# Kernel optimization log

Hardware: AMD Instinct MI355X
Metric: run time of the kernel (lower is better)

Reference implementation:

```python
import jax, jax.numpy as jnp
import numpy as np

NF = 64        # num_feat
B = 4
H = 128
W = 128
KH = KW = 3
K = KH * KW    # 9 kernel taps
DG = 1         # deformable_groups


def conv3x3(x, w, b):
    y = jax.lax.conv_general_dilated(
        x, w, window_strides=(1, 1), padding=((1, 1), (1, 1)),
        dimension_numbers=('NCHW', 'OIHW', 'NCHW'))
    return y + b[None, :, None, None]


def lrelu(x):
    return jnp.where(x >= 0, x, 0.1 * x)


def modulated_deform_conv(x, offset, mask, w, b):
    """DCNv2: bilinear gather at learned offsets, modulated by sigmoid mask.
    x: [B,C,H,W], offset: [B,2K,H,W] (y,x interleaved per tap), mask: [B,K,H,W].
    stride=1, padding=1, dilation=1, zero outside boundaries (mmcv semantics).
    """
    Bb, C, Hh, Ww = x.shape
    off = offset.reshape(Bb, K, 2, Hh, Ww)
    oy, ox = off[:, :, 0], off[:, :, 1]
    ki = (jnp.arange(K) // KW - 1).astype(x.dtype)  # dilation*i - pad
    kj = (jnp.arange(K) % KW - 1).astype(x.dtype)
    py = jnp.arange(Hh, dtype=x.dtype)[None, None, :, None] + ki[None, :, None, None] + oy  # [B,K,H,W]
    px = jnp.arange(Ww, dtype=x.dtype)[None, None, None, :] + kj[None, :, None, None] + ox
    y0 = jnp.floor(py)
    x0 = jnp.floor(px)
    wy1 = py - y0
    wx1 = px - x0
    x_flat = x.reshape(Bb, C, Hh * Ww)

    def gather(yi, xi):
        valid = (yi >= 0) & (yi < Hh) & (xi >= 0) & (xi < Ww)
        yc = jnp.clip(yi, 0, Hh - 1).astype(jnp.int32)
        xc = jnp.clip(xi, 0, Ww - 1).astype(jnp.int32)
        idx = (yc * Ww + xc).reshape(Bb, -1)                      # [B, K*H*W]
        g = jax.vmap(lambda xf, i: jnp.take(xf, i, axis=1))(x_flat, idx)  # [B,C,K*H*W]
        g = g.reshape(Bb, C, K, Hh, Ww)
        return g * valid[:, None].astype(x.dtype)

    v00 = gather(y0, x0)
    v01 = gather(y0, x0 + 1)
    v10 = gather(y0 + 1, x0)
    v11 = gather(y0 + 1, x0 + 1)
    wy = wy1[:, None]
    wx = wx1[:, None]
    samp = (v00 * (1 - wy) * (1 - wx) + v01 * (1 - wy) * wx
            + v10 * wy * (1 - wx) + v11 * wy * wx)                # [B,C,K,H,W]
    samp = samp * mask[:, None]
    out = jnp.einsum('bckhw,ock->bohw', samp, w.reshape(w.shape[0], C, K))
    return out + b[None, :, None, None]


def setup_inputs() -> dict:
    key = jax.random.key(0)
    ks = jax.random.split(key, 12)
    s = 0.05
    return {
        'nbr_feat_l': jax.random.normal(ks[0], (B, NF, H, W), jnp.float32),
        'ref_feat_l': jax.random.normal(ks[1], (B, NF, H, W), jnp.float32),
        'w1': jax.random.normal(ks[2], (NF, 2 * NF, 3, 3), jnp.float32) * s,
        'b1': jnp.zeros((NF,), jnp.float32),
        'w2': jax.random.normal(ks[3], (NF, NF, 3, 3), jnp.float32) * s,
        'b2': jnp.zeros((NF,), jnp.float32),
        'w3': jax.random.normal(ks[4], (NF, NF, 3, 3), jnp.float32) * s,
        'b3': jnp.zeros((NF,), jnp.float32),
        'w_off': jax.random.normal(ks[5], (DG * 3 * K, NF, 3, 3), jnp.float32) * s,
        'b_off': jnp.zeros((DG * 3 * K,), jnp.float32),
        'w_dcn': jax.random.normal(ks[6], (NF, NF, 3, 3), jnp.float32) * s,
        'b_dcn': jnp.zeros((NF,), jnp.float32),
    }


def reference(nbr_feat_l, ref_feat_l, w1, b1, w2, b2, w3, b3, w_off, b_off, w_dcn, b_dcn):
    o = jnp.concatenate([nbr_feat_l, ref_feat_l], axis=1)
    o = lrelu(conv3x3(o, w1, b1))
    o = lrelu(conv3x3(o, w2, b2))
    o = lrelu(conv3x3(o, w3, b3))
    out = conv3x3(o, w_off, b_off)                      # [B, 27, H, W]
    o1, o2, m = jnp.split(out, 3, axis=1)
    offset = 15 * jnp.tanh(jnp.concatenate([o1, o2], axis=1))  # [B, 18, H, W]
    mask = jax.nn.sigmoid(m)                                   # [B, 9, H, W]
    feat = lrelu(modulated_deform_conv(nbr_feat_l, offset, mask, w_dcn, b_dcn))
    return feat, offset, mask
```

## Files before the change

kernel.cpp:

```cpp
#include <hip/hip_runtime.h>
#include <math.h>


typedef _Float16 h8 __attribute__((ext_vector_type(8)));
typedef _Float16 h4 __attribute__((ext_vector_type(4)));
typedef _Float16 h2 __attribute__((ext_vector_type(2)));
typedef float f4 __attribute__((ext_vector_type(4)));

__global__ __launch_bounds__(256) void setup_kernel(
    const float* __restrict__ nbr, const float* __restrict__ refp,
    const float* __restrict__ w1, const float* __restrict__ w2,
    const float* __restrict__ w3, const float* __restrict__ w_off,
    const float* __restrict__ w_dcn,
    _Float16* __restrict__ X1, _Float16* __restrict__ X2,
    _Float16* __restrict__ B64, _Float16* __restrict__ C64,
    _Float16* __restrict__ wF1, _Float16* __restrict__ wF2,
    _Float16* __restrict__ wF3, _Float16* __restrict__ wFo,
    _Float16* __restrict__ wFd) {
  __shared__ float t[64 * 65];
  int bid = blockIdx.x;
  int tid = threadIdx.x;
  if (bid < 792) {
    int i = bid * 256 + tid;
    if (i < 73728) {
      int j = i;
      int icw = j & 31; int t1 = j >> 5; int oc = t1 & 63; int t2 = t1 >> 6;
      int ch = t2 & 3; int tap = t2 >> 2; int ic = ch * 32 + icw;
      wF1[j] = (_Float16)w1[(oc * 128 + ic) * 9 + tap];
    } else if (i < 110592) {
      int j = i - 73728;
      int icw = j & 31; int t1 = j >> 5; int oc = t1 & 63; int t2 = t1 >> 6;
      int ch = t2 & 1; int tap = t2 >> 1; int ic = ch * 32 + icw;
      wF2[j] = (_Float16)w2[(oc * 64 + ic) * 9 + tap];
    } else if (i < 147456) {
      int j = i - 110592;
      int icw = j & 31; int t1 = j >> 5; int oc = t1 & 63; int t2 = t1 >> 6;
      int ch = t2 & 1; int tap = t2 >> 1; int ic = ch * 32 + icw;
      wF3[j] = (_Float16)w3[(oc * 64 + ic) * 9 + tap];
    } else if (i < 165888) {
      int j = i - 147456;
      int icw = j & 31; int t1 = j >> 5; int oc = t1 & 31; int t2 = t1 >> 5;
      int ch = t2 & 1; int tap = t2 >> 1; int ic = ch * 32 + icw;
      float v = (oc < 27) ? w_off[(oc * 64 + ic) * 9 + tap] : 0.f;
      wFo[j] = (_Float16)v;
    } else if (i < 202752) {
      int j = i - 165888;
      int oc = j / 576; int r = j - oc * 576; int tap = r >> 6; int c = r & 63;
      wFd[j] = (_Float16)w_dcn[(oc * 64 + c) * 9 + tap];
    }
    return;
  }
  if (bid < 1050) {
    int i = (bid - 792) * 256 + tid;
    int bufi = i / 16512;
    int j = i - bufi * 16512;
    int b = j / 4128;
    int r = j - b * 4128;
    int p = r >> 3; int cg = r & 7;
    int row, col;
    if (p < 130)      { row = 0;   col = p; }
    else if (p < 260) { row = 129; col = p - 130; }
    else if (p < 388) { row = 1 + (p - 260); col = 0; }
    else              { row = 1 + (p - 388); col = 129; }
    _Float16* dst = (bufi == 0) ? X1 : (bufi == 1) ? X2 : (bufi == 2) ? B64 : C64;
    uint4 z; z.x = z.y = z.z = z.w = 0u;
    *(uint4*)(dst + ((size_t)(b * 130 + row) * 130 + col) * 64 + cg * 8) = z;
    return;
  }
  int j = bid - 1050;
  int half = j & 1;
  int y = (j >> 1) & 127;
  int b = (j >> 8) & 3;
  int src = j >> 10;
  const float* sp = src ? refp : nbr;
  _Float16* dst = src ? X2 : X1;
  for (int l = tid; l < 64 * 64; l += 256) {
    int c = l >> 6, gx = l & 63;
    t[c * 65 + gx] = sp[(((size_t)b * 64 + c) << 14) + (y << 7) + half * 64 + gx];
  }
  __syncthreads();
  unsigned* dstU = (unsigned*)dst;
  for (int l = tid; l < 64 * 32; l += 256) {
    int pxl = l >> 5, c2 = l & 31;
    union { _Float16 h[2]; unsigned u; } pk;
    pk.h[0] = (_Float16)t[(2 * c2) * 65 + pxl];
    pk.h[1] = (_Float16)t[(2 * c2 + 1) * 65 + pxl];
    dstU[((size_t)(b * 130 + y + 1) * 130 + 1 + half * 64 + pxl) * 32 + c2] = pk.u;
  }
}

template <int NCH, bool SPLIT>
__global__ __launch_bounds__(128, 1) void conv3x3_w64_kernel(
    const _Float16* __restrict__ X1, const _Float16* __restrict__ X2,
    const _Float16* __restrict__ W, const float* __restrict__ bias,
    _Float16* __restrict__ outP) {
  int tid = threadIdx.x;
  int wv = tid >> 6, L = tid & 63;
  int lm = L & 15, lq = L >> 4;
  int bid = blockIdx.x;
  int xcd = bid & 7, j = bid >> 3;
  int y = (xcd << 4) | (j & 15);
  int b = j >> 4;
  int px0 = wv * 64;

  f4 acc[4][4];
#pragma unroll
  for (int i = 0; i < 4; ++i)
#pragma unroll
    for (int n = 0; n < 4; ++n) acc[i][n] = (f4)0.f;

#pragma unroll
  for (int c = 0; c < NCH; ++c) {
    const _Float16* src = (SPLIT && c >= 2) ? X2 : X1;
    int cl = SPLIT ? (c & 1) : c;
#pragma unroll
    for (int tap = 0; tap < 9; ++tap) {
      const int dy = tap / 3 - 1, dx = tap % 3 - 1;
      const _Float16* xb = src + ((size_t)((b * 130 + (y + 1 + dy)) * 130) + (1 + dx) + px0) * 64
                               + cl * 32 + lq * 8;
      h8 b0 = *(const h8*)(xb + lm * 64);
      h8 b1 = *(const h8*)(xb + (16 + lm) * 64);
      h8 b2 = *(const h8*)(xb + (32 + lm) * 64);
      h8 b3 = *(const h8*)(xb + (48 + lm) * 64);
      const _Float16* wp = W + (size_t)((tap * NCH + c) * 64) * 32 + lm * 32 + lq * 8;
      h8 a0 = *(const h8*)(wp);
      h8 a1 = *(const h8*)(wp + 512);
      h8 a2 = *(const h8*)(wp + 1024);
      h8 a3 = *(const h8*)(wp + 1536);
#pragma unroll
      for (int mt = 0; mt < 4; ++mt) {
        h8 am = (mt == 0) ? a0 : (mt == 1) ? a1 : (mt == 2) ? a2 : a3;
        acc[mt][0] = __builtin_amdgcn_mfma_f32_16x16x32_f16(am, b0, acc[mt][0], 0, 0, 0);
        acc[mt][1] = __builtin_amdgcn_mfma_f32_16x16x32_f16(am, b1, acc[mt][1], 0, 0, 0);
        acc[mt][2] = __builtin_amdgcn_mfma_f32_16x16x32_f16(am, b2, acc[mt][2], 0, 0, 0);
        acc[mt][3] = __builtin_amdgcn_mfma_f32_16x16x32_f16(am, b3, acc[mt][3], 0, 0, 0);
      }
    }
  }
  const size_t obase = ((size_t)(b * 130 + (y + 1)) * 130 + 1) * 64;
#pragma unroll
  for (int mt = 0; mt < 4; ++mt)
#pragma unroll
    for (int nt = 0; nt < 4; ++nt) {
      int px = px0 + nt * 16 + lm;
      h4 pk;
#pragma unroll
      for (int r = 0; r < 4; ++r) {
        int oc = mt * 16 + lq * 4 + r;
        float v = acc[mt][nt][r] + bias[oc];
        v = (v >= 0.f) ? v : 0.1f * v;
        pk[r] = (_Float16)v;
      }
      *(h4*)(outP + obase + (size_t)px * 64 + mt * 16 + lq * 4) = pk;
    }
}

__global__ __launch_bounds__(256, 8) void off_dcn_kernel(
    const _Float16* __restrict__ Xc, const _Float16* __restrict__ Xs,
    const _Float16* __restrict__ Wo, const float* __restrict__ bo,
    const _Float16* __restrict__ wD, const float* __restrict__ bd,
    float* __restrict__ off_out, float* __restrict__ mask_out,
    float* __restrict__ out) {
  __shared__ _Float16 S[32 * 200];
  __shared__ float Soff[32][28];
  int tid = threadIdx.x;
  int wv = tid >> 6, L = tid & 63;
  int lm = L & 15, lq = L >> 4;
  int t8 = L >> 3, c8 = L & 7;
  int g = blockIdx.x;
  int xcd = g & 7;
  int r0 = g >> 3;
  int q = r0 & 3;
  int y = (xcd << 4) | ((r0 >> 2) & 15);
  int b = r0 >> 6;
  int pxq0 = q * 32;

  if (wv < 2) {
    int px0 = pxq0 + wv * 16;
    f4 oa[2];
    oa[0] = (f4)0.f; oa[1] = (f4)0.f;
#pragma unroll
    for (int c = 0; c < 2; ++c)
#pragma unroll
      for (int tap = 0; tap < 9; ++tap) {
        const int dy = tap / 3 - 1, dx = tap % 3 - 1;
        const _Float16* xb = Xc + ((size_t)((b * 130 + (y + 1 + dy)) * 130) + (1 + dx) + px0) * 64
                                + c * 32 + lq * 8;
        h8 b0 = *(const h8*)(xb + lm * 64);
        const _Float16* wp = Wo + (size_t)((tap * 2 + c) * 32 + lm) * 32 + lq * 8;
        h8 a0 = *(const h8*)(wp);
        h8 a1 = *(const h8*)(wp + 512);
        oa[0] = __builtin_amdgcn_mfma_f32_16x16x32_f16(a0, b0, oa[0], 0, 0, 0);
        oa[1] = __builtin_amdgcn_mfma_f32_16x16x32_f16(a1, b0, oa[1], 0, 0, 0);
      }
    int gpx = px0 + lm;
    int hw = (y << 7) + gpx;
    int lpx = wv * 16 + lm;
#pragma unroll
    for (int mt = 0; mt < 2; ++mt)
#pragma unroll
      for (int r = 0; r < 4; ++r) {
        int oc = mt * 16 + lq * 4 + r;
        if (oc < 18) {
          float v = 15.f * tanhf(oa[mt][r] + bo[oc]);
          off_out[((b * 18 + oc) << 14) + hw] = v;
          Soff[lpx][oc] = v;
        } else if (oc < 27) {
          float v = 1.f / (1.f + expf(-(oa[mt][r] + bo[oc])));
          mask_out[((b * 9 + (oc - 18)) << 14) + hw] = v;
          Soff[lpx][oc] = v;
        }
      }
  }

  f4 acc[2];
  acc[0] = (f4)0.f; acc[1] = (f4)0.f;
  int wvM = wv >> 1, wvN = wv & 1;

#pragma unroll
  for (int p = 0; p < 3; ++p) {
    const int tap0 = p * 3;
    __syncthreads();
#pragma unroll
    for (int it = 0; it < 3; ++it) {
      int u = it * 32 + wv * 8 + t8;
      int px = u & 31;
      int tl = u >> 5;
      int k = tap0 + tl;
      int wg = pxq0 + px;
      int kr = k / 3;
      float oy = Soff[px][2 * k];
      float ox = Soff[px][2 * k + 1];
      float m = Soff[px][18 + k];
      float py = (float)(y + kr - 1) + oy;
      float pxf = (float)(wg + (k - kr * 3) - 1) + ox;
      float fy = floorf(py), fx = floorf(pxf);
      float wy = py - fy, wx = pxf - fx;
      int y0 = (int)fy, x0 = (int)fx;
      int y1 = y0 + 1, x1 = x0 + 1;
      float vy0 = ((unsigned)y0 < 128u) ? 1.f : 0.f;
      float vy1 = ((unsigned)y1 < 128u) ? 1.f : 0.f;
      float vx0 = ((unsigned)x0 < 128u) ? 1.f : 0.f;
      float vx1 = ((unsigned)x1 < 128u) ? 1.f : 0.f;
      float ey = 1.f - wy, ex = 1.f - wx;
      _Float16 w00 = (_Float16)(ey * ex * m * vy0 * vx0);
      _Float16 w01 = (_Float16)(ey * wx * m * vy0 * vx1);
      _Float16 w10 = (_Float16)(wy * ex * m * vy1 * vx0);
      _Float16 w11 = (_Float16)(wy * wx * m * vy1 * vx1);
      h2 W00 = {w00, w00}, W01 = {w01, w01}, W10 = {w10, w10}, W11 = {w11, w11};
      int y0c = min(max(y0, 0), 127) + 1, y1c = min(max(y1, 0), 127) + 1;
      int x0c = min(max(x0, 0), 127) + 1, x1c = min(max(x1, 0), 127) + 1;
      int rb = b * 130;
      h8 v00 = *(const h8*)(Xs + ((size_t)((rb + y0c) * 130 + x0c) << 6) + c8 * 8);
      h8 v01 = *(const h8*)(Xs + ((size_t)((rb + y0c) * 130 + x1c) << 6) + c8 * 8);
      h8 v10 = *(const h8*)(Xs + ((size_t)((rb + y1c) * 130 + x0c) << 6) + c8 * 8);
      h8 v11 = *(const h8*)(Xs + ((size_t)((rb + y1c) * 130 + x1c) << 6) + c8 * 8);
      h8 o;
#pragma unroll
      for (int j2 = 0; j2 < 4; ++j2) {
        h2 a = {v00[2 * j2], v00[2 * j2 + 1]};
        h2 bb = {v01[2 * j2], v01[2 * j2 + 1]};
        h2 cc = {v10[2 * j2], v10[2 * j2 + 1]};
        h2 dd = {v11[2 * j2], v11[2 * j2 + 1]};
        h2 r = a * W00;
        r += bb * W01;
        r += cc * W10;
        r += dd * W11;
        o[2 * j2] = r[0];
        o[2 * j2 + 1] = r[1];
      }
      *(h8*)&S[px * 200 + tl * 64 + c8 * 8] = o;
    }
    __syncthreads();
#pragma unroll
    for (int ks = 0; ks < 6; ++ks) {
      int kg = tap0 * 64 + ks * 32;
      const _Float16* wp = wD + (size_t)(wvM * 32 + lm) * 576 + kg + lq * 8;
      h8 a0 = *(const h8*)(wp);
      h8 a1 = *(const h8*)(wp + 16 * 576);
      h8 bv = *(const h8*)(&S[(wvN * 16 + lm) * 200 + ks * 32 + lq * 8]);
      acc[0] = __builtin_amdgcn_mfma_f32_16x16x32_f16(a0, bv, acc[0], 0, 0, 0);
      acc[1] = __builtin_amdgcn_mfma_f32_16x16x32_f16(a1, bv, acc[1], 0, 0, 0);
    }
  }
  int px = pxq0 + wvN * 16 + lm;
#pragma unroll
  for (int mt = 0; mt < 2; ++mt)
#pragma unroll
    for (int r = 0; r < 4; ++r) {
      int oc = wvM * 32 + mt * 16 + lq * 4 + r;
      float v = acc[mt][r] + bd[oc];
      v = (v >= 0.f) ? v : 0.1f * v;
      out[(((b << 6) + oc) << 14) + (y << 7) + px] = v;
    }
}

extern "C" void kernel_launch(void* const* d_in, const int* in_sizes, int n_in,
                              void* d_out, int out_size, void* d_ws, size_t ws_size,
                              hipStream_t stream) {
  const float* nbr   = (const float*)d_in[0];
  const float* refp  = (const float*)d_in[1];
  const float* w1    = (const float*)d_in[2];
  const float* b1    = (const float*)d_in[3];
  const float* w2    = (const float*)d_in[4];
  const float* b2    = (const float*)d_in[5];
  const float* w3    = (const float*)d_in[6];
  const float* b3    = (const float*)d_in[7];
  const float* w_off = (const float*)d_in[8];
  const float* b_off = (const float*)d_in[9];
  const float* w_dcn = (const float*)d_in[10];
  const float* b_dcn = (const float*)d_in[11];

  float* outp = (float*)d_out;
  float* feat = outp;
  float* offp = outp + 4194304;
  float* mskp = outp + 4194304 + 1179648;

  char* ws = (char*)d_ws;
  const size_t PB = 8652800;
  _Float16* X1  = (_Float16*)ws;
  _Float16* X2  = (_Float16*)(ws + PB);
  _Float16* B64 = (_Float16*)(ws + 2 * PB);
  _Float16* C64 = (_Float16*)(ws + 3 * PB);
  char* p = ws + 4 * PB;
  _Float16* wF1 = (_Float16*)p;  p += (size_t)73728 * 2;
  _Float16* wF2 = (_Float16*)p;  p += (size_t)36864 * 2;
  _Float16* wF3 = (_Float16*)p;  p += (size_t)36864 * 2;
  _Float16* wFo = (_Float16*)p;  p += (size_t)18432 * 2;
  _Float16* wFd = (_Float16*)p;

  setup_kernel<<<dim3(3098), 256, 0, stream>>>(nbr, refp, w1, w2, w3, w_off, w_dcn,
                                               X1, X2, B64, C64, wF1, wF2, wF3, wFo, wFd);
  conv3x3_w64_kernel<4, true><<<dim3(512), 128, 0, stream>>>(X1, X2, wF1, b1, B64);
  conv3x3_w64_kernel<2, false><<<dim3(512), 128, 0, stream>>>(B64, nullptr, wF2, b2, C64);
  conv3x3_w64_kernel<2, false><<<dim3(512), 128, 0, stream>>>(C64, nullptr, wF3, b3, B64);
  off_dcn_kernel<<<dim3(2048), 256, 0, stream>>>(B64, X1, wFo, b_off, wFd, b_dcn,
                                                 offp, mskp, feat);
}
```

Baseline: 228.9 us.

## Split conv output channels across blocks and spread offset conv over all waves

The three 3x3 conv kernels now split the 64 output channels into two halves per block and use four waves of 32 pixels each. This doubles the grid to 1024 blocks of 256 threads, with a 2x2 MFMA tile per wave instead of 4x4. The offset/mask conv in the fused DCN kernel is now spread across all four waves, each computing one 16-channel half for 16 pixels, instead of only two waves doing both halves. The goal is more parallelism and occupancy and less register pressure per wave. The cost is less data reuse per wave, so input pixels and weights are loaded more often. The launch-bounds occupancy hint on the DCN kernel is also lowered.

```diff
diff --git a/kernel.cpp b/kernel.cpp
--- a/kernel.cpp
+++ b/kernel.cpp
@@ -90,7 +90,7 @@
 }
 
 template <int NCH, bool SPLIT>
-__global__ __launch_bounds__(128, 1) void conv3x3_w64_kernel(
+__global__ __launch_bounds__(256, 4) void conv3x3_w32_kernel(
     const _Float16* __restrict__ X1, const _Float16* __restrict__ X2,
     const _Float16* __restrict__ W, const float* __restrict__ bias,
     _Float16* __restrict__ outP) {
@@ -99,15 +99,16 @@
   int lm = L & 15, lq = L >> 4;
   int bid = blockIdx.x;
   int xcd = bid & 7, j = bid >> 3;
-  int y = (xcd << 4) | (j & 15);
-  int b = j >> 4;
-  int px0 = wv * 64;
-
-  f4 acc[4][4];
-#pragma unroll
-  for (int i = 0; i < 4; ++i)
-#pragma unroll
-    for (int n = 0; n < 4; ++n) acc[i][n] = (f4)0.f;
+  int och = j & 1;
+  int y = (xcd << 4) | ((j >> 1) & 15);
+  int b = j >> 5;
+  int px0 = wv * 32;
+
+  f4 acc[2][2];
+#pragma unroll
+  for (int i = 0; i < 2; ++i)
+#pragma unroll
+    for (int n = 0; n < 2; ++n) acc[i][n] = (f4)0.f;
 
 #pragma unroll
   for (int c = 0; c < NCH; ++c) {
@@ -120,42 +121,34 @@
                                + cl * 32 + lq * 8;
       h8 b0 = *(const h8*)(xb + lm * 64);
       h8 b1 = *(const h8*)(xb + (16 + lm) * 64);
-      h8 b2 = *(const h8*)(xb + (32 + lm) * 64);
-      h8 b3 = *(const h8*)(xb + (48 + lm) * 64);
-      const _Float16* wp = W + (size_t)((tap * NCH + c) * 64) * 32 + lm * 32 + lq * 8;
+      const _Float16* wp = W + (size_t)((tap * NCH + c) * 64 + och * 32 + lm) * 32 + lq * 8;
       h8 a0 = *(const h8*)(wp);
       h8 a1 = *(const h8*)(wp + 512);
-      h8 a2 = *(const h8*)(wp + 1024);
-      h8 a3 = *(const h8*)(wp + 1536);
-#pragma unroll
-      for (int mt = 0; mt < 4; ++mt) {
-        h8 am = (mt == 0) ? a0 : (mt == 1) ? a1 : (mt == 2) ? a2 : a3;
-        acc[mt][0] = __builtin_amdgcn_mfma_f32_16x16x32_f16(am, b0, acc[mt][0], 0, 0, 0);
-        acc[mt][1] = __builtin_amdgcn_mfma_f32_16x16x32_f16(am, b1, acc[mt][1], 0, 0, 0);
-        acc[mt][2] = __builtin_amdgcn_mfma_f32_16x16x32_f16(am, b2, acc[mt][2], 0, 0, 0);
-        acc[mt][3] = __builtin_amdgcn_mfma_f32_16x16x32_f16(am, b3, acc[mt][3], 0, 0, 0);
-      }
+      acc[0][0] = __builtin_amdgcn_mfma_f32_16x16x32_f16(a0, b0, acc[0][0], 0, 0, 0);
+      acc[0][1] = __builtin_amdgcn_mfma_f32_16x16x32_f16(a0, b1, acc[0][1], 0, 0, 0);
+      acc[1][0] = __builtin_amdgcn_mfma_f32_16x16x32_f16(a1, b0, acc[1][0], 0, 0, 0);
+      acc[1][1] = __builtin_amdgcn_mfma_f32_16x16x32_f16(a1, b1, acc[1][1], 0, 0, 0);
     }
   }
   const size_t obase = ((size_t)(b * 130 + (y + 1)) * 130 + 1) * 64;
 #pragma unroll
-  for (int mt = 0; mt < 4; ++mt)
-#pragma unroll
-    for (int nt = 0; nt < 4; ++nt) {
+  for (int mt = 0; mt < 2; ++mt)
+#pragma unroll
+    for (int nt = 0; nt < 2; ++nt) {
       int px = px0 + nt * 16 + lm;
       h4 pk;
 #pragma unroll
       for (int r = 0; r < 4; ++r) {
-        int oc = mt * 16 + lq * 4 + r;
+        int oc = och * 32 + mt * 16 + lq * 4 + r;
         float v = acc[mt][nt][r] + bias[oc];
         v = (v >= 0.f) ? v : 0.1f * v;
         pk[r] = (_Float16)v;
       }
-      *(h4*)(outP + obase + (size_t)px * 64 + mt * 16 + lq * 4) = pk;
+      *(h4*)(outP + obase + (size_t)px * 64 + och * 32 + mt * 16 + lq * 4) = pk;
     }
 }
 
-__global__ __launch_bounds__(256, 8) void off_dcn_kernel(
+__global__ __launch_bounds__(256, 4) void off_dcn_kernel(
     const _Float16* __restrict__ Xc, const _Float16* __restrict__ Xs,
     const _Float16* __restrict__ Wo, const float* __restrict__ bo,
     const _Float16* __restrict__ wD, const float* __restrict__ bd,
@@ -175,10 +168,10 @@
   int b = r0 >> 6;
   int pxq0 = q * 32;
 
-  if (wv < 2) {
-    int px0 = pxq0 + wv * 16;
-    f4 oa[2];
-    oa[0] = (f4)0.f; oa[1] = (f4)0.f;
+  {
+    int pxh = wv & 1, oh = wv >> 1;
+    int px0 = pxq0 + pxh * 16;
+    f4 oa = (f4)0.f;
 #pragma unroll
     for (int c = 0; c < 2; ++c)
 #pragma unroll
@@ -187,30 +180,26 @@
         const _Float16* xb = Xc + ((size_t)((b * 130 + (y + 1 + dy)) * 130) + (1 + dx) + px0) * 64
                                 + c * 32 + lq * 8;
         h8 b0 = *(const h8*)(xb + lm * 64);
-        const _Float16* wp = Wo + (size_t)((tap * 2 + c) * 32 + lm) * 32 + lq * 8;
+        const _Float16* wp = Wo + (size_t)((tap * 2 + c) * 32 + oh * 16 + lm) * 32 + lq * 8;
         h8 a0 = *(const h8*)(wp);
-        h8 a1 = *(const h8*)(wp + 512);
-        oa[0] = __builtin_amdgcn_mfma_f32_16x16x32_f16(a0, b0, oa[0], 0, 0, 0);
-        oa[1] = __builtin_amdgcn_mfma_f32_16x16x32_f16(a1, b0, oa[1], 0, 0, 0);
+        oa = __builtin_amdgcn_mfma_f32_16x16x32_f16(a0, b0, oa, 0, 0, 0);
       }
     int gpx = px0 + lm;
     int hw = (y << 7) + gpx;
-    int lpx = wv * 16 + lm;
-#pragma unroll
-    for (int mt = 0; mt < 2; ++mt)
-#pragma unroll
-      for (int r = 0; r < 4; ++r) {
-        int oc = mt * 16 + lq * 4 + r;
-        if (oc < 18) {
-          float v = 15.f * tanhf(oa[mt][r] + bo[oc]);
-          off_out[((b * 18 + oc) << 14) + hw] = v;
-          Soff[lpx][oc] = v;
-        } else if (oc < 27) {
-          float v = 1.f / (1.f + expf(-(oa[mt][r] + bo[oc])));
-          mask_out[((b * 9 + (oc - 18)) << 14) + hw] = v;
-          Soff[lpx][oc] = v;
-        }
+    int lpx = pxh * 16 + lm;
+#pragma unroll
+    for (int r = 0; r < 4; ++r) {
+      int oc = oh * 16 + lq * 4 + r;
+      if (oc < 18) {
+        float v = 15.f * tanhf(oa[r] + bo[oc]);
+        off_out[((b * 18 + oc) << 14) + hw] = v;
+        Soff[lpx][oc] = v;
+      } else if (oc < 27) {
+        float v = 1.f / (1.f + expf(-(oa[r] + bo[oc])));
+        mask_out[((b * 9 + (oc - 18)) << 14) + hw] = v;
+        Soff[lpx][oc] = v;
       }
+    }
   }
 
   f4 acc[2];
@@ -331,9 +320,9 @@
 
   setup_kernel<<<dim3(3098), 256, 0, stream>>>(nbr, refp, w1, w2, w3, w_off, w_dcn,
                                                X1, X2, B64, C64, wF1, wF2, wF3, wFo, wFd);
-  conv3x3_w64_kernel<4, true><<<dim3(512), 128, 0, stream>>>(X1, X2, wF1, b1, B64);
-  conv3x3_w64_kernel<2, false><<<dim3(512), 128, 0, stream>>>(B64, nullptr, wF2, b2, C64);
-  conv3x3_w64_kernel<2, false><<<dim3(512), 128, 0, stream>>>(C64, nullptr, wF3, b3, B64);
+  conv3x3_w32_kernel<4, true><<<dim3(1024), 256, 0, stream>>>(X1, X2, wF1, b1, B64);
+  conv3x3_w32_kernel<2, false><<<dim3(1024), 256, 0, stream>>>(B64, nullptr, wF2, b2, C64);
+  conv3x3_w32_kernel<2, false><<<dim3(1024), 256, 0, stream>>>(C64, nullptr, wF3, b3, B64);
   off_dcn_kernel<<<dim3(2048), 256, 0, stream>>>(B64, X1, wFo, b_off, wFd, b_dcn,
                                                  offp, mskp, feat);
 }
```

New measurement: 274.1 us. 1.2x slower.

## Fuse DCN sampling directly into MFMA operands per wave, removing shared staging

Applied to the files above, without the earlier changes.

Each block now covers 64 pixels, and every wave owns 16 of them end to end. The wave computes the offset conv for its pixels, then builds the bilinear-sampled B operand in registers and feeds it straight into MFMAs over all 64 output channels. This removes the shared-memory sample tile and the block-wide barriers between sampling and the GEMM, and all four waves now do offset-conv work instead of two. The cost is more accumulators per wave (4 f4 instead of 2), which is why launch bounds drop to 4 blocks per CU. The grid is also halved, so there is less parallelism to hide gather latency.

```diff
diff --git a/kernel.cpp b/kernel.cpp
--- a/kernel.cpp
+++ b/kernel.cpp
@@ -155,28 +155,29 @@
     }
 }
 
-__global__ __launch_bounds__(256, 8) void off_dcn_kernel(
+__global__ __launch_bounds__(256, 4) void off_dcn_kernel(
     const _Float16* __restrict__ Xc, const _Float16* __restrict__ Xs,
     const _Float16* __restrict__ Wo, const float* __restrict__ bo,
     const _Float16* __restrict__ wD, const float* __restrict__ bd,
     float* __restrict__ off_out, float* __restrict__ mask_out,
     float* __restrict__ out) {
-  __shared__ _Float16 S[32 * 200];
-  __shared__ float Soff[32][28];
+  __shared__ float Soff[4][16][28];
   int tid = threadIdx.x;
   int wv = tid >> 6, L = tid & 63;
   int lm = L & 15, lq = L >> 4;
-  int t8 = L >> 3, c8 = L & 7;
+  int lq8 = lq * 8;
   int g = blockIdx.x;
   int xcd = g & 7;
   int r0 = g >> 3;
-  int q = r0 & 3;
-  int y = (xcd << 4) | ((r0 >> 2) & 15);
-  int b = r0 >> 6;
-  int pxq0 = q * 32;
-
-  if (wv < 2) {
-    int px0 = pxq0 + wv * 16;
+  int half = r0 & 1;
+  int y = (xcd << 4) | ((r0 >> 1) & 15);
+  int b = r0 >> 5;
+  int px0 = half * 64 + wv * 16;
+  int gpx = px0 + lm;
+  int hw = (y << 7) + gpx;
+  int rb = b * 130;
+
+  {
     f4 oa[2];
     oa[0] = (f4)0.f; oa[1] = (f4)0.f;
 #pragma unroll
@@ -184,18 +185,15 @@
 #pragma unroll
       for (int tap = 0; tap < 9; ++tap) {
         const int dy = tap / 3 - 1, dx = tap % 3 - 1;
-        const _Float16* xb = Xc + ((size_t)((b * 130 + (y + 1 + dy)) * 130) + (1 + dx) + px0) * 64
-                                + c * 32 + lq * 8;
+        const _Float16* xb = Xc + ((size_t)((rb + (y + 1 + dy)) * 130) + (1 + dx) + px0) * 64
+                                + c * 32 + lq8;
         h8 b0 = *(const h8*)(xb + lm * 64);
-        const _Float16* wp = Wo + (size_t)((tap * 2 + c) * 32 + lm) * 32 + lq * 8;
+        const _Float16* wp = Wo + (size_t)((tap * 2 + c) * 32 + lm) * 32 + lq8;
         h8 a0 = *(const h8*)(wp);
         h8 a1 = *(const h8*)(wp + 512);
         oa[0] = __builtin_amdgcn_mfma_f32_16x16x32_f16(a0, b0, oa[0], 0, 0, 0);
         oa[1] = __builtin_amdgcn_mfma_f32_16x16x32_f16(a1, b0, oa[1], 0, 0, 0);
       }
-    int gpx = px0 + lm;
-    int hw = (y << 7) + gpx;
-    int lpx = wv * 16 + lm;
 #pragma unroll
     for (int mt = 0; mt < 2; ++mt)
 #pragma unroll
@@ -204,61 +202,57 @@
         if (oc < 18) {
           float v = 15.f * tanhf(oa[mt][r] + bo[oc]);
           off_out[((b * 18 + oc) << 14) + hw] = v;
-          Soff[lpx][oc] = v;
+          Soff[wv][lm][oc] = v;
         } else if (oc < 27) {
           float v = 1.f / (1.f + expf(-(oa[mt][r] + bo[oc])));
           mask_out[((b * 9 + (oc - 18)) << 14) + hw] = v;
-          Soff[lpx][oc] = v;
+          Soff[wv][lm][oc] = v;
         }
       }
   }
 
-  f4 acc[2];
-  acc[0] = (f4)0.f; acc[1] = (f4)0.f;
-  int wvM = wv >> 1, wvN = wv & 1;
-
-#pragma unroll
-  for (int p = 0; p < 3; ++p) {
-    const int tap0 = p * 3;
-    __syncthreads();
-#pragma unroll
-    for (int it = 0; it < 3; ++it) {
-      int u = it * 32 + wv * 8 + t8;
-      int px = u & 31;
-      int tl = u >> 5;
-      int k = tap0 + tl;
-      int wg = pxq0 + px;
-      int kr = k / 3;
-      float oy = Soff[px][2 * k];
-      float ox = Soff[px][2 * k + 1];
-      float m = Soff[px][18 + k];
-      float py = (float)(y + kr - 1) + oy;
-      float pxf = (float)(wg + (k - kr * 3) - 1) + ox;
-      float fy = floorf(py), fx = floorf(pxf);
-      float wy = py - fy, wx = pxf - fx;
-      int y0 = (int)fy, x0 = (int)fx;
-      int y1 = y0 + 1, x1 = x0 + 1;
-      float vy0 = ((unsigned)y0 < 128u) ? 1.f : 0.f;
-      float vy1 = ((unsigned)y1 < 128u) ? 1.f : 0.f;
-      float vx0 = ((unsigned)x0 < 128u) ? 1.f : 0.f;
-      float vx1 = ((unsigned)x1 < 128u) ? 1.f : 0.f;
-      float ey = 1.f - wy, ex = 1.f - wx;
-      _Float16 w00 = (_Float16)(ey * ex * m * vy0 * vx0);
-      _Float16 w01 = (_Float16)(ey * wx * m * vy0 * vx1);
-      _Float16 w10 = (_Float16)(wy * ex * m * vy1 * vx0);
-      _Float16 w11 = (_Float16)(wy * wx * m * vy1 * vx1);
-      h2 W00 = {w00, w00}, W01 = {w01, w01}, W10 = {w10, w10}, W11 = {w11, w11};
-      int y0c = min(max(y0, 0), 127) + 1, y1c = min(max(y1, 0), 127) + 1;
-      int x0c = min(max(x0, 0), 127) + 1, x1c = min(max(x1, 0), 127) + 1;
-      int rb = b * 130;
-      h8 v00 = *(const h8*)(Xs + ((size_t)((rb + y0c) * 130 + x0c) << 6) + c8 * 8);
-      h8 v01 = *(const h8*)(Xs + ((size_t)((rb + y0c) * 130 + x1c) << 6) + c8 * 8);
-      h8 v10 = *(const h8*)(Xs + ((size_t)((rb + y1c) * 130 + x0c) << 6) + c8 * 8);
-      h8 v11 = *(const h8*)(Xs + ((size_t)((rb + y1c) * 130 + x1c) << 6) + c8 * 8);
-      h8 o;
+  f4 acc[4];
+#pragma unroll
+  for (int m = 0; m < 4; ++m) acc[m] = (f4)0.f;
+
+#pragma unroll
+  for (int k = 0; k < 9; ++k) {
+    const int kr = k / 3, kc = k - kr * 3;
+    float oy = Soff[wv][lm][2 * k];
+    float ox = Soff[wv][lm][2 * k + 1];
+    float m = Soff[wv][lm][18 + k];
+    float py = (float)(y + kr - 1) + oy;
+    float pxf = (float)(gpx + kc - 1) + ox;
+    float fy = floorf(py), fx = floorf(pxf);
+    float wy = py - fy, wx = pxf - fx;
+    int y0 = (int)fy, x0 = (int)fx;
+    int y1 = y0 + 1, x1 = x0 + 1;
+    float vy0 = ((unsigned)y0 < 128u) ? 1.f : 0.f;
+    float vy1 = ((unsigned)y1 < 128u) ? 1.f : 0.f;
+    float vx0 = ((unsigned)x0 < 128u) ? 1.f : 0.f;
+    float vx1 = ((unsigned)x1 < 128u) ? 1.f : 0.f;
+    float ey = 1.f - wy, ex = 1.f - wx;
+    _Float16 w00 = (_Float16)(ey * ex * m * vy0 * vx0);
+    _Float16 w01 = (_Float16)(ey * wx * m * vy0 * vx1);
+    _Float16 w10 = (_Float16)(wy * ex * m * vy1 * vx0);
+    _Float16 w11 = (_Float16)(wy * wx * m * vy1 * vx1);
+    h2 W00 = {w00, w00}, W01 = {w01, w01}, W10 = {w10, w10}, W11 = {w11, w11};
+    int y0c = min(max(y0, 0), 127) + 1, y1c = min(max(y1, 0), 127) + 1;
+    int x0c = min(max(x0, 0), 127) + 1, x1c = min(max(x1, 0), 127) + 1;
+    const _Float16* r0p = Xs + (((size_t)((rb + y0c) * 130)) << 6);
+    const _Float16* r1p = Xs + (((size_t)((rb + y1c) * 130)) << 6);
+    int c0 = x0c << 6, c1 = x1c << 6;
+#pragma unroll
+    for (int s = 0; s < 2; ++s) {
+      int cb = s * 32 + lq8;
+      h8 v00 = *(const h8*)(r0p + c0 + cb);
+      h8 v01 = *(const h8*)(r0p + c1 + cb);
+      h8 v10 = *(const h8*)(r1p + c0 + cb);
+      h8 v11 = *(const h8*)(r1p + c1 + cb);
+      h8 bv;
 #pragma unroll
       for (int j2 = 0; j2 < 4; ++j2) {
-        h2 a = {v00[2 * j2], v00[2 * j2 + 1]};
+        h2 a  = {v00[2 * j2], v00[2 * j2 + 1]};
         h2 bb = {v01[2 * j2], v01[2 * j2 + 1]};
         h2 cc = {v10[2 * j2], v10[2 * j2 + 1]};
         h2 dd = {v11[2 * j2], v11[2 * j2 + 1]};
@@ -266,32 +260,25 @@
         r += bb * W01;
         r += cc * W10;
         r += dd * W11;
-        o[2 * j2] = r[0];
-        o[2 * j2 + 1] = r[1];
-      }
-      *(h8*)&S[px * 200 + tl * 64 + c8 * 8] = o;
-    }
-    __syncthreads();
-#pragma unroll
-    for (int ks = 0; ks < 6; ++ks) {
-      int kg = tap0 * 64 + ks * 32;
-      const _Float16* wp = wD + (size_t)(wvM * 32 + lm) * 576 + kg + lq * 8;
-      h8 a0 = *(const h8*)(wp);
-      h8 a1 = *(const h8*)(wp + 16 * 576);
-      h8 bv = *(const h8*)(&S[(wvN * 16 + lm) * 200 + ks * 32 + lq * 8]);
-      acc[0] = __builtin_amdgcn_mfma_f32_16x16x32_f16(a0, bv, acc[0], 0, 0, 0);
-      acc[1] = __builtin_amdgcn_mfma_f32_16x16x32_f16(a1, bv, acc[1], 0, 0, 0);
-    }
-  }
-  int px = pxq0 + wvN * 16 + lm;
-#pragma unroll
-  for (int mt = 0; mt < 2; ++mt)
+        bv[2 * j2] = r[0];
+        bv[2 * j2 + 1] = r[1];
+      }
+      const _Float16* wp = wD + (size_t)lm * 576 + k * 64 + cb;
+      acc[0] = __builtin_amdgcn_mfma_f32_16x16x32_f16(*(const h8*)(wp), bv, acc[0], 0, 0, 0);
+      acc[1] = __builtin_amdgcn_mfma_f32_16x16x32_f16(*(const h8*)(wp + 16 * 576), bv, acc[1], 0, 0, 0);
+      acc[2] = __builtin_amdgcn_mfma_f32_16x16x32_f16(*(const h8*)(wp + 32 * 576), bv, acc[2], 0, 0, 0);
+      acc[3] = __builtin_amdgcn_mfma_f32_16x16x32_f16(*(const h8*)(wp + 48 * 576), bv, acc[3], 0, 0, 0);
+    }
+  }
+
+#pragma unroll
+  for (int m = 0; m < 4; ++m)
 #pragma unroll
     for (int r = 0; r < 4; ++r) {
-      int oc = wvM * 32 + mt * 16 + lq * 4 + r;
-      float v = acc[mt][r] + bd[oc];
+      int oc = m * 16 + lq * 4 + r;
+      float v = acc[m][r] + bd[oc];
       v = (v >= 0.f) ? v : 0.1f * v;
-      out[(((b << 6) + oc) << 14) + (y << 7) + px] = v;
+      out[(((b << 6) + oc) << 14) + (y << 7) + gpx] = v;
     }
 }
 
@@ -334,6 +321,6 @@
   conv3x3_w64_kernel<4, true><<<dim3(512), 128, 0, stream>>>(X1, X2, wF1, b1, B64);
   conv3x3_w64_kernel<2, false><<<dim3(512), 128, 0, stream>>>(B64, nullptr, wF2, b2, C64);
   conv3x3_w64_kernel<2, false><<<dim3(512), 128, 0, stream>>>(C64, nullptr, wF3, b3, B64);
-  off_dcn_kernel<<<dim3(2048), 256, 0, stream>>>(B64, X1, wFo, b_off, wFd, b_dcn,
+  off_dcn_kernel<<<dim3(1024), 256, 0, stream>>>(B64, X1, wFo, b_off, wFd, b_dcn,
                                                  offp, mskp, feat);
 }
```

Result: slower. 246.0 us (+7.5%).
